# Kernel optimization log

Measured on AMD Instinct MI355X. Metric: run time of the kernel, lower is better.

Reference implementation:

```python
import jax, jax.numpy as jnp
import numpy as np
from jax.ops import segment_sum

N_NODES = 10000
N_EDGES = 320000


def leaky_relu(x):
    return jnp.where(x >= 0, x, 0.01 * x)


def gcn_layer(edge_h, src, dst, W, b):
    # (1) node h = mean of incoming edge features
    deg = segment_sum(jnp.ones((edge_h.shape[0],), edge_h.dtype), dst, num_segments=N_NODES)
    deg = jnp.maximum(deg, 1.0)
    h = segment_sum(edge_h, dst, num_segments=N_NODES) / deg[:, None]
    # (2) update_all: node h = sum over in-edges of src node h
    h2 = segment_sum(h[src], dst, num_segments=N_NODES)
    # (3) edge h = mean of endpoint node features
    eh = 0.5 * (h2[src] + h2[dst])
    # (4) linear on edge features
    return eh @ W.T + b


def setup_inputs() -> dict:
    key = jax.random.key(0)
    ks = jax.random.split(key, 20)
    d_in, d_h, d_out = 128, 256, 64
    inp = {
        'inputs1': jax.random.normal(ks[0], (N_EDGES, d_in), jnp.float32),
        'src1': jax.random.randint(ks[1], (N_EDGES,), 0, N_NODES, jnp.int32),
        'dst1': jax.random.randint(ks[2], (N_EDGES,), 0, N_NODES, jnp.int32),
        'inputs2': jax.random.normal(ks[3], (N_EDGES, d_in), jnp.float32),
        'src2': jax.random.randint(ks[4], (N_EDGES,), 0, N_NODES, jnp.int32),
        'dst2': jax.random.randint(ks[5], (N_EDGES,), 0, N_NODES, jnp.int32),
        'W11': jax.random.normal(ks[6], (d_h, d_in), jnp.float32) * 0.05,
        'b11': jax.random.normal(ks[7], (d_h,), jnp.float32) * 0.05,
        'W12': jax.random.normal(ks[8], (d_h, d_h), jnp.float32) * 0.05,
        'b12': jax.random.normal(ks[9], (d_h,), jnp.float32) * 0.05,
        'W21': jax.random.normal(ks[10], (d_h, d_in), jnp.float32) * 0.05,
        'b21': jax.random.normal(ks[11], (d_h,), jnp.float32) * 0.05,
        'W22': jax.random.normal(ks[12], (d_h, d_h), jnp.float32) * 0.05,
        'b22': jax.random.normal(ks[13], (d_h,), jnp.float32) * 0.05,
        'W3': jax.random.normal(ks[14], (d_out, 2 * d_h), jnp.float32) * 0.05,
        'b3': jax.random.normal(ks[15], (d_out,), jnp.float32) * 0.05,
    }
    return inp


def reference(inputs1, src1, dst1, inputs2, src2, dst2,
              W11, b11, W12, b12, W21, b21, W22, b22, W3, b3):
    h1 = leaky_relu(gcn_layer(inputs1, src1, dst1, W11, b11))
    h1 = leaky_relu(gcn_layer(h1, src1, dst1, W12, b12))
    h1 = jnp.mean(h1, axis=0)
    h2 = leaky_relu(gcn_layer(inputs2, src2, dst2, W21, b21))
    h2 = leaky_relu(gcn_layer(h2, src2, dst2, W22, b22))
    h2 = jnp.mean(h2, axis=0)
    out = jnp.concatenate((h1, h2), axis=0)
    return out @ W3.T + b3
```

## Files before the change

kernel.cpp:

```cpp
#include <hip/hip_runtime.h>
#include <cstddef>

#define NN 10000
#define NB 2500

typedef unsigned int u32;
typedef unsigned short u16;
typedef __attribute__((ext_vector_type(8))) short short8;
typedef __attribute__((ext_vector_type(4))) float f32x4;

__device__ __forceinline__ float lrelu(float x) { return x >= 0.f ? x : 0.01f * x; }

__device__ __forceinline__ float bf_lo(u32 v) { union { u32 i; float f; } c; c.i = v << 16; return c.f; }
__device__ __forceinline__ float bf_hi(u32 v) { union { u32 i; float f; } c; c.i = v & 0xFFFF0000u; return c.f; }
__device__ __forceinline__ u32 rne_bits(float f) {
  union { float f; u32 i; } c; c.f = f;
  return c.i + 0x7FFFu + ((c.i >> 16) & 1u);
}
__device__ __forceinline__ u32 pack2(float a, float b) {
  return (rne_bits(a) >> 16) | (rne_bits(b) & 0xFFFF0000u);
}

__global__ __launch_bounds__(256) void wconv_kernel(
    const float* __restrict__ a, const float* __restrict__ b,
    const float* __restrict__ c, const float* __restrict__ d,
    u16* __restrict__ oa, u16* __restrict__ ob,
    u16* __restrict__ oc, u16* __restrict__ od,
    int* __restrict__ degbase ) {
  int i = blockIdx.x * 256 + threadIdx.x;
  if (i < 32768) oa[i] = (u16)(rne_bits(a[i]) >> 16);
  else if (i < 98304) ob[i - 32768] = (u16)(rne_bits(b[i - 32768]) >> 16);
  else if (i < 131072) oc[i - 98304] = (u16)(rne_bits(c[i - 98304]) >> 16);
  else if (i < 196608) od[i - 131072] = (u16)(rne_bits(d[i - 131072]) >> 16);
  if (i < 4 * NN) degbase[i] = 0;
}

__global__ __launch_bounds__(256) void count_b_kernel(const int* __restrict__ dstA,
                                                      const int* __restrict__ dstB,
                                                      int* __restrict__ degbase, int E) {
  const int g = blockIdx.y;
  const int* dst = g ? dstB : dstA;
  int* degi = degbase + (size_t)g * 2 * NN;
  int e = blockIdx.x * 256 + threadIdx.x;
  if (e < E) atomicAdd(&degi[dst[e]], 1);
}

__global__ __launch_bounds__(1024) void scan_b_kernel(const int* __restrict__ degbase,
                                                      int* __restrict__ offbase,
                                                      float* __restrict__ rdegbase, int n) {
  const int g = blockIdx.x;
  const int* degi = degbase + (size_t)g * 2 * NN;
  int* off = offbase + (size_t)g * NN;
  float* rdeg = rdegbase + (size_t)g * NN;
  __shared__ int wsum[16];
  __shared__ int wpre[16];
  __shared__ int carry_s;
  const int tid = threadIdx.x;
  const int lane = tid & 63, w = tid >> 6;
  if (tid == 0) carry_s = 0;
  __syncthreads();
  for (int base = 0; base < n; base += 1024) {
    int i = base + tid;
    int x = (i < n) ? degi[i] : 0;
    int v = x;
#pragma unroll
    for (int d = 1; d < 64; d <<= 1) {
      int t = __shfl_up(v, d);
      if (lane >= d) v += t;
    }
    if (lane == 63) wsum[w] = v;
    __syncthreads();
    if (tid == 0) {
      int s = carry_s;
#pragma unroll
      for (int j = 0; j < 16; ++j) { int t = wsum[j]; wpre[j] = s; s += t; }
      carry_s = s;
    }
    __syncthreads();
    if (i < n) {
      off[i] = wpre[w] + (v - x);
      rdeg[i] = 1.0f / fmaxf((float)x, 1.0f);
    }
    __syncthreads();
  }
}

__global__ __launch_bounds__(256) void scatterA_b_kernel(
    const float* __restrict__ featA, const float* __restrict__ featB,
    const int* __restrict__ srcA, const int* __restrict__ dstA,
    const int* __restrict__ srcB, const int* __restrict__ dstB,
    const int* __restrict__ offbase, int* __restrict__ degbase,
    u32* __restrict__ tmpb , int* __restrict__ esrc_sb, int E) {
  const int g = blockIdx.y;
  const float* feat = g ? featB : featA;
  const int* src = g ? srcB : srcA;
  const int* dst = g ? dstB : dstA;
  const int* off = offbase + (size_t)g * NN;
  int* cursor = degbase + (size_t)g * 2 * NN + NN;
  u32* tmp = tmpb + (size_t)g * E * 64;
  int* esrc_s = esrc_sb + (size_t)g * E;
  const int idx = blockIdx.x * 8 + (threadIdx.x >> 5);
  const int lane32 = threadIdx.x & 31;
  if (idx >= E) return;
  int p0 = 0, sv = 0;
  if (lane32 == 0) {
    const int dv = dst[idx];
    sv = src[idx];
    p0 = off[dv] + atomicAdd(&cursor[dv], 1);
  }
  const int p = __shfl(p0, threadIdx.x & 32);
  const float4 v = *(const float4*)&feat[(size_t)idx * 128 + (lane32 << 2)];
  uint2 o;
  o.x = pack2(v.x, v.y);
  o.y = pack2(v.z, v.w);
  *(uint2*)&tmp[(size_t)p * 64 + (lane32 << 1)] = o;
  if (lane32 == 0) esrc_s[p] = sv;
}

__global__ __launch_bounds__(256) void reduceA_b_kernel(
    const u32* __restrict__ tmpb, const int* __restrict__ offbase,
    const int* __restrict__ degbase, const float* __restrict__ rdegbase,
    u32* __restrict__ outbfb , int E) {
  const int g = blockIdx.y;
  const u32* tmp = tmpb + (size_t)g * E * 64;
  const int* off = offbase + (size_t)g * NN;
  const int* degi = degbase + (size_t)g * 2 * NN;
  const float* rdeg = rdegbase + (size_t)g * NN;
  u32* outbf = outbfb + (size_t)g * NN * 64;
  const int n = (blockIdx.x << 2) + (threadIdx.x >> 6);
  const int lane = threadIdx.x & 63;
  const int hl = lane & 31, h = lane >> 5;
  const int o = off[n], d = degi[n];
  const u32* basep = tmp + (size_t)o * 64 + (hl << 1);
  float4 acc = make_float4(0.f, 0.f, 0.f, 0.f);
  int j = h;
  for (; j + 6 < d; j += 8) {
    const uint2 v0 = *(const uint2*)(basep + (size_t)j * 64);
    const uint2 v1 = *(const uint2*)(basep + (size_t)(j + 2) * 64);
    const uint2 v2 = *(const uint2*)(basep + (size_t)(j + 4) * 64);
    const uint2 v3 = *(const uint2*)(basep + (size_t)(j + 6) * 64);
    acc.x += (bf_lo(v0.x) + bf_lo(v1.x)) + (bf_lo(v2.x) + bf_lo(v3.x));
    acc.y += (bf_hi(v0.x) + bf_hi(v1.x)) + (bf_hi(v2.x) + bf_hi(v3.x));
    acc.z += (bf_lo(v0.y) + bf_lo(v1.y)) + (bf_lo(v2.y) + bf_lo(v3.y));
    acc.w += (bf_hi(v0.y) + bf_hi(v1.y)) + (bf_hi(v2.y) + bf_hi(v3.y));
  }
  for (; j < d; j += 2) {
    const uint2 v0 = *(const uint2*)(basep + (size_t)j * 64);
    acc.x += bf_lo(v0.x); acc.y += bf_hi(v0.x);
    acc.z += bf_lo(v0.y); acc.w += bf_hi(v0.y);
  }
  acc.x += __shfl(acc.x, lane ^ 32);
  acc.y += __shfl(acc.y, lane ^ 32);
  acc.z += __shfl(acc.z, lane ^ 32);
  acc.w += __shfl(acc.w, lane ^ 32);
  if (h == 0) {
    const float sc = rdeg[n];
    uint2 r;
    r.x = pack2(acc.x * sc, acc.y * sc);
    r.y = pack2(acc.z * sc, acc.w * sc);
    *(uint2*)&outbf[(size_t)n * 64 + (hl << 1)] = r;
  }
}

__global__ __launch_bounds__(256) void gatherB_b_kernel(
    const u32* __restrict__ featb , const int* __restrict__ gidxb,
    const int* __restrict__ offbase, const int* __restrict__ degbase,
    u32* __restrict__ outbfb, int E) {
  const int bid = blockIdx.x;
  const int r = bid & 7, t = bid >> 3;
  const int g = r >> 2;
  const int nb = t * 4 + (r & 3);
  const u32* feat = featb + (size_t)g * NN * 64;
  const int* gidx = gidxb + (size_t)g * E;
  const int* off = offbase + (size_t)g * NN;
  const int* degi = degbase + (size_t)g * 2 * NN;
  u32* outbf = outbfb + (size_t)g * NN * 64;
  const int n = (nb << 2) + (threadIdx.x >> 6);
  const int lane = threadIdx.x & 63;
  const int hl = lane & 31, h = lane >> 5;
  const int o = off[n], d = degi[n];
  const int fo = hl << 1;
  float4 acc = make_float4(0.f, 0.f, 0.f, 0.f);
  for (int c0 = 0; c0 < d; c0 += 64) {
    const int m = min(64, d - c0);
    const int gg = (lane < m) ? gidx[o + c0 + lane] : 0;
    const int pairs = m >> 1;
    int i = 0;
    for (; i + 4 <= pairs; i += 4) {
      const int e0 = 2 * i + h;
      const int s0 = __shfl(gg, e0), s1 = __shfl(gg, e0 + 2);
      const int s2 = __shfl(gg, e0 + 4), s3 = __shfl(gg, e0 + 6);
      const uint2 v0 = *(const uint2*)&feat[(s0 << 6) + fo];
      const uint2 v1 = *(const uint2*)&feat[(s1 << 6) + fo];
      const uint2 v2 = *(const uint2*)&feat[(s2 << 6) + fo];
      const uint2 v3 = *(const uint2*)&feat[(s3 << 6) + fo];
      acc.x += (bf_lo(v0.x) + bf_lo(v1.x)) + (bf_lo(v2.x) + bf_lo(v3.x));
      acc.y += (bf_hi(v0.x) + bf_hi(v1.x)) + (bf_hi(v2.x) + bf_hi(v3.x));
      acc.z += (bf_lo(v0.y) + bf_lo(v1.y)) + (bf_lo(v2.y) + bf_lo(v3.y));
      acc.w += (bf_hi(v0.y) + bf_hi(v1.y)) + (bf_hi(v2.y) + bf_hi(v3.y));
    }
    for (; i < pairs; ++i) {
      const int s0 = __shfl(gg, 2 * i + h);
      const uint2 v0 = *(const uint2*)&feat[(s0 << 6) + fo];
      acc.x += bf_lo(v0.x); acc.y += bf_hi(v0.x);
      acc.z += bf_lo(v0.y); acc.w += bf_hi(v0.y);
    }
    if (m & 1) {
      const int s0 = __shfl(gg, m - 1);
      const float wgt = (h == 0) ? 1.f : 0.f;
      const uint2 v0 = *(const uint2*)&feat[(s0 << 6) + fo];
      acc.x = fmaf(bf_lo(v0.x), wgt, acc.x);
      acc.y = fmaf(bf_hi(v0.x), wgt, acc.y);
      acc.z = fmaf(bf_lo(v0.y), wgt, acc.z);
      acc.w = fmaf(bf_hi(v0.y), wgt, acc.w);
    }
  }
  acc.x += __shfl(acc.x, lane ^ 32);
  acc.y += __shfl(acc.y, lane ^ 32);
  acc.z += __shfl(acc.z, lane ^ 32);
  acc.w += __shfl(acc.w, lane ^ 32);
  if (h == 0) {
    uint2 r2;
    r2.x = pack2(acc.x, acc.y);
    r2.y = pack2(acc.z, acc.w);
    *(uint2*)&outbf[(size_t)n * 64 + (hl << 1)] = r2;
  }
}

__device__ __forceinline__ void acc_bf4(float4& a, uint2 v, const float4& zn, const float4& bb) {
  a.x += lrelu(0.5f * (bf_lo(v.x) + zn.x) + bb.x);
  a.y += lrelu(0.5f * (bf_hi(v.x) + zn.y) + bb.y);
  a.z += lrelu(0.5f * (bf_lo(v.y) + zn.z) + bb.z);
  a.w += lrelu(0.5f * (bf_hi(v.y) + zn.w) + bb.w);
}

__global__ __launch_bounds__(256) void passC_b_kernel(
    const u32* __restrict__ Zb_, const int* __restrict__ esrcb,
    const int* __restrict__ offbase, const int* __restrict__ degbase,
    const float* __restrict__ rdegbase,
    const float* __restrict__ biasA, const float* __restrict__ biasB,
    u32* __restrict__ hBb, int E) {
  const int bid = blockIdx.x;
  const int r = bid & 7, t = bid >> 3;
  const int g = r >> 2, fh = (r >> 1) & 1;
  const int nb = t * 2 + (r & 1);
  const u32* Z = Zb_ + (size_t)g * NN * 128;
  const int* esrc = esrcb + (size_t)g * E;
  const int* off = offbase + (size_t)g * NN;
  const int* degi = degbase + (size_t)g * 2 * NN;
  const float* rdeg = rdegbase + (size_t)g * NN;
  const float* bias = g ? biasB : biasA;
  u32* hB = hBb + (size_t)g * NN * 128;
  const int n = (nb << 2) + (threadIdx.x >> 6);
  const int lane = threadIdx.x & 63;
  const int hl = lane & 31, h = lane >> 5;
  const int o = off[n], d = degi[n];
  const int fo = (fh << 6) + (hl << 1);
  const uint2 znv = *(const uint2*)&Z[(n << 7) + fo];
  const float4 zn = make_float4(bf_lo(znv.x), bf_hi(znv.x), bf_lo(znv.y), bf_hi(znv.y));
  const float4 bb = *(const float4*)&bias[(fh << 7) + (hl << 2)];
  float4 a = make_float4(0.f, 0.f, 0.f, 0.f);
  for (int c0 = 0; c0 < d; c0 += 64) {
    const int m = min(64, d - c0);
    const int gg = (lane < m) ? esrc[o + c0 + lane] : 0;
    const int pairs = m >> 1;
    int i = 0;
    for (; i + 4 <= pairs; i += 4) {
      const int e0 = 2 * i + h;
      const int s0 = __shfl(gg, e0), s1 = __shfl(gg, e0 + 2);
      const int s2 = __shfl(gg, e0 + 4), s3 = __shfl(gg, e0 + 6);
      const uint2 z0 = *(const uint2*)&Z[(s0 << 7) + fo];
      const uint2 z1 = *(const uint2*)&Z[(s1 << 7) + fo];
      const uint2 z2 = *(const uint2*)&Z[(s2 << 7) + fo];
      const uint2 z3 = *(const uint2*)&Z[(s3 << 7) + fo];
      acc_bf4(a, z0, zn, bb);
      acc_bf4(a, z1, zn, bb);
      acc_bf4(a, z2, zn, bb);
      acc_bf4(a, z3, zn, bb);
    }
    for (; i < pairs; ++i) {
      const int s0 = __shfl(gg, 2 * i + h);
      const uint2 z0 = *(const uint2*)&Z[(s0 << 7) + fo];
      acc_bf4(a, z0, zn, bb);
    }
    if (m & 1) {
      const int s0 = __shfl(gg, m - 1);
      const uint2 z0 = *(const uint2*)&Z[(s0 << 7) + fo];
      if (h == 0) acc_bf4(a, z0, zn, bb);
    }
  }
  a.x += __shfl(a.x, lane ^ 32); a.y += __shfl(a.y, lane ^ 32);
  a.z += __shfl(a.z, lane ^ 32); a.w += __shfl(a.w, lane ^ 32);
  if (h == 0) {
    const float rr = rdeg[n];
    uint2 outv;
    outv.x = pack2(a.x * rr, a.y * rr);
    outv.y = pack2(a.z * rr, a.w * rr);
    *(uint2*)&hB[(n << 7) + fo] = outv;
  }
}

__global__ __launch_bounds__(256) void gatherC_b_kernel(
    const u32* __restrict__ featb , const int* __restrict__ gidxb,
    const int* __restrict__ offbase, const int* __restrict__ degbase,
    u32* __restrict__ outbfb, int E) {
  const int bid = blockIdx.x;
  const int r = bid & 7, t = bid >> 3;
  const int g = r >> 2, fh = (r >> 1) & 1;
  const int nb = t * 2 + (r & 1);
  const u32* feat = featb + (size_t)g * NN * 128;
  const int* gidx = gidxb + (size_t)g * E;
  const int* off = offbase + (size_t)g * NN;
  const int* degi = degbase + (size_t)g * 2 * NN;
  u32* outbf = outbfb + (size_t)g * NN * 128;
  const int n = (nb << 2) + (threadIdx.x >> 6);
  const int lane = threadIdx.x & 63;
  const int hl = lane & 31, h = lane >> 5;
  const int o = off[n], d = degi[n];
  const int fo = (fh << 6) + (hl << 1);
  float4 a = make_float4(0.f, 0.f, 0.f, 0.f);
  for (int c0 = 0; c0 < d; c0 += 64) {
    const int m = min(64, d - c0);
    const int gg = (lane < m) ? gidx[o + c0 + lane] : 0;
    const int pairs = m >> 1;
    int i = 0;
    for (; i + 4 <= pairs; i += 4) {
      const int e0 = 2 * i + h;
      const int s0 = __shfl(gg, e0), s1 = __shfl(gg, e0 + 2);
      const int s2 = __shfl(gg, e0 + 4), s3 = __shfl(gg, e0 + 6);
      const uint2 z0 = *(const uint2*)&feat[(s0 << 7) + fo];
      const uint2 z1 = *(const uint2*)&feat[(s1 << 7) + fo];
      const uint2 z2 = *(const uint2*)&feat[(s2 << 7) + fo];
      const uint2 z3 = *(const uint2*)&feat[(s3 << 7) + fo];
      a.x += (bf_lo(z0.x) + bf_lo(z1.x)) + (bf_lo(z2.x) + bf_lo(z3.x));
      a.y += (bf_hi(z0.x) + bf_hi(z1.x)) + (bf_hi(z2.x) + bf_hi(z3.x));
      a.z += (bf_lo(z0.y) + bf_lo(z1.y)) + (bf_lo(z2.y) + bf_lo(z3.y));
      a.w += (bf_hi(z0.y) + bf_hi(z1.y)) + (bf_hi(z2.y) + bf_hi(z3.y));
    }
    for (; i < pairs; ++i) {
      const int s0 = __shfl(gg, 2 * i + h);
      const uint2 z0 = *(const uint2*)&feat[(s0 << 7) + fo];
      a.x += bf_lo(z0.x); a.y += bf_hi(z0.x);
      a.z += bf_lo(z0.y); a.w += bf_hi(z0.y);
    }
    if (m & 1) {
      const int s0 = __shfl(gg, m - 1);
      const uint2 z0 = *(const uint2*)&feat[(s0 << 7) + fo];
      if (h == 0) {
        a.x += bf_lo(z0.x); a.y += bf_hi(z0.x);
        a.z += bf_lo(z0.y); a.w += bf_hi(z0.y);
      }
    }
  }
  a.x += __shfl(a.x, lane ^ 32); a.y += __shfl(a.y, lane ^ 32);
  a.z += __shfl(a.z, lane ^ 32); a.w += __shfl(a.w, lane ^ 32);
  if (h == 0) {
    uint2 outv;
    outv.x = pack2(a.x, a.y);
    outv.y = pack2(a.z, a.w);
    *(uint2*)&outbf[(n << 7) + fo] = outv;
  }
}

__global__ __launch_bounds__(256) void passE_b_kernel(
    const u32* __restrict__ Z2b, const int* __restrict__ esrcb,
    const int* __restrict__ offbase, const int* __restrict__ degbase,
    const float* __restrict__ biasA, const float* __restrict__ biasB,
    float* __restrict__ partialsb , int nNodes, int E) {
  const int bid = blockIdx.x;
  const int r = bid & 7, t = bid >> 3;
  const int g = r >> 2, fh = (r >> 1) & 1;
  const int blk = t * 2 + (r & 1);
  const u32* Z2 = Z2b + (size_t)g * NN * 128;
  const int* esrc = esrcb + (size_t)g * E;
  const int* off = offbase + (size_t)g * NN;
  const int* degi = degbase + (size_t)g * 2 * NN;
  const float* bias = g ? biasB : biasA;
  float* partials = partialsb + (size_t)((g * 2 + fh) * 128 + blk) * 128;
  const int lane = threadIdx.x & 63, w = threadIdx.x >> 6;
  const int hl = lane & 31, h = lane >> 5;
  const int fo = (fh << 6) + (hl << 1);
  const float4 bb = *(const float4*)&bias[(fh << 7) + (hl << 2)];
  float4 a = make_float4(0.f, 0.f, 0.f, 0.f);
  for (int n = blk * 4 + w; n < nNodes; n += 512) {
    const int o = off[n], d = degi[n];
    const uint2 znv = *(const uint2*)&Z2[(n << 7) + fo];
    const float4 zn = make_float4(bf_lo(znv.x), bf_hi(znv.x), bf_lo(znv.y), bf_hi(znv.y));
    for (int c0 = 0; c0 < d; c0 += 64) {
      const int m = min(64, d - c0);
      const int gg = (lane < m) ? esrc[o + c0 + lane] : 0;
      const int pairs = m >> 1;
      int i = 0;
      for (; i + 4 <= pairs; i += 4) {
        const int e0 = 2 * i + h;
        const int s0 = __shfl(gg, e0), s1 = __shfl(gg, e0 + 2);
        const int s2 = __shfl(gg, e0 + 4), s3 = __shfl(gg, e0 + 6);
        const uint2 z0 = *(const uint2*)&Z2[(s0 << 7) + fo];
        const uint2 z1 = *(const uint2*)&Z2[(s1 << 7) + fo];
        const uint2 z2 = *(const uint2*)&Z2[(s2 << 7) + fo];
        const uint2 z3 = *(const uint2*)&Z2[(s3 << 7) + fo];
        acc_bf4(a, z0, zn, bb);
        acc_bf4(a, z1, zn, bb);
        acc_bf4(a, z2, zn, bb);
        acc_bf4(a, z3, zn, bb);
      }
      for (; i < pairs; ++i) {
        const int s0 = __shfl(gg, 2 * i + h);
        const uint2 z0 = *(const uint2*)&Z2[(s0 << 7) + fo];
        acc_bf4(a, z0, zn, bb);
      }
      if (m & 1) {
        const int s0 = __shfl(gg, m - 1);
        const uint2 z0 = *(const uint2*)&Z2[(s0 << 7) + fo];
        if (h == 0) acc_bf4(a, z0, zn, bb);
      }
    }
  }
  a.x += __shfl(a.x, lane ^ 32); a.y += __shfl(a.y, lane ^ 32);
  a.z += __shfl(a.z, lane ^ 32); a.w += __shfl(a.w, lane ^ 32);
  __shared__ float red[4][128];
  if (h == 0) *(float4*)&red[w][hl << 2] = a;
  __syncthreads();
  const int tid = threadIdx.x;
  if (tid < 128) partials[tid] = red[0][tid] + red[1][tid] + red[2][tid] + red[3][tid];
}

__global__ __launch_bounds__(1024) void final_fused_kernel(
    const float* __restrict__ partialsb ,
    const float* __restrict__ W3, const float* __restrict__ b3,
    float* __restrict__ out, float invE) {
  __shared__ float smacc[512];
  __shared__ float tmp2[2][512];
  __shared__ float red[16][64];
  const int tid = threadIdx.x;
  {
    const int half = tid >> 9;
    const int q = tid & 511;
    const float* basep = partialsb + (size_t)(q >> 7) * 128 * 128 + (q & 127);
    float s = 0.f;
    for (int b = half * 64; b < half * 64 + 64; ++b) s += basep[(size_t)b * 128];
    tmp2[half][q] = s;
  }
  __syncthreads();
  if (tid < 512) smacc[tid] = tmp2[0][tid] + tmp2[1][tid];
  __syncthreads();
  const int j = tid & 63, part = tid >> 6;
  float acc = 0.f;
  for (int kk = 0; kk < 32; ++kk) {
    const int k = part * 32 + kk;
    acc += smacc[k] * W3[(size_t)j * 512 + k];
  }
  red[part][j] = acc;
  __syncthreads();
  if (part == 0) {
    float s = 0.f;
#pragma unroll
    for (int p = 0; p < 16; ++p) s += red[p][j];
    out[j] = b3[j] + s * invE;
  }
}

template <int K>
__global__ __launch_bounds__(256) void gemm_mfma_b_kernel(const u16* __restrict__ Ab,
                                                          const u16* __restrict__ WA,
                                                          const u16* __restrict__ WB,
                                                          u16* __restrict__ Cb, int N) {
  const int g = blockIdx.z;
  const u16* A = Ab + (size_t)g * NN * K;
  const u16* Wb = g ? WB : WA;
  u16* C = Cb + (size_t)g * NN * 256;
  const int lane = threadIdx.x & 63;
  const int w = threadIdx.x >> 6;
  const int wm = w >> 1, wn = w & 1;
  const int bn = blockIdx.x * 64 + wm * 32;
  const int bo = blockIdx.y * 64 + wn * 32;
  const int r0 = lane & 15;
  const int kq = lane >> 4;
  const int ra0 = min(bn + r0, N - 1);
  const int ra1 = min(bn + 16 + r0, N - 1);
  const u16* a0p = &A[(size_t)ra0 * K + kq * 8];
  const u16* a1p = &A[(size_t)ra1 * K + kq * 8];
  const u16* b0p = &Wb[(size_t)(bo + r0) * K + kq * 8];
  const u16* b1p = &Wb[(size_t)(bo + 16 + r0) * K + kq * 8];
  f32x4 acc00 = {0.f, 0.f, 0.f, 0.f}, acc01 = {0.f, 0.f, 0.f, 0.f};
  f32x4 acc10 = {0.f, 0.f, 0.f, 0.f}, acc11 = {0.f, 0.f, 0.f, 0.f};
#pragma unroll
  for (int k0 = 0; k0 < K; k0 += 32) {
    const short8 a0 = *(const short8*)(a0p + k0);
    const short8 a1 = *(const short8*)(a1p + k0);
    const short8 b0 = *(const short8*)(b0p + k0);
    const short8 b1 = *(const short8*)(b1p + k0);
    acc00 = __builtin_amdgcn_mfma_f32_16x16x32_bf16(a0, b0, acc00, 0, 0, 0);
    acc01 = __builtin_amdgcn_mfma_f32_16x16x32_bf16(a0, b1, acc01, 0, 0, 0);
    acc10 = __builtin_amdgcn_mfma_f32_16x16x32_bf16(a1, b0, acc10, 0, 0, 0);
    acc11 = __builtin_amdgcn_mfma_f32_16x16x32_bf16(a1, b1, acc11, 0, 0, 0);
  }
#pragma unroll
  for (int r = 0; r < 4; ++r) {
    const int n0 = bn + 4 * kq + r;
    if (n0 < N) {
      C[(size_t)n0 * 256 + bo + r0] = (u16)(rne_bits(acc00[r]) >> 16);
      C[(size_t)n0 * 256 + bo + 16 + r0] = (u16)(rne_bits(acc01[r]) >> 16);
    }
    const int n1 = bn + 16 + 4 * kq + r;
    if (n1 < N) {
      C[(size_t)n1 * 256 + bo + r0] = (u16)(rne_bits(acc10[r]) >> 16);
      C[(size_t)n1 * 256 + bo + 16 + r0] = (u16)(rne_bits(acc11[r]) >> 16);
    }
  }
}

extern "C" void kernel_launch(void* const* d_in, const int* in_sizes, int n_in,
                              void* d_out, int out_size, void* d_ws, size_t ws_size,
                              hipStream_t stream) {
  const float* in1 = (const float*)d_in[0];
  const int* src1 = (const int*)d_in[1];
  const int* dst1 = (const int*)d_in[2];
  const float* in2 = (const float*)d_in[3];
  const int* src2 = (const int*)d_in[4];
  const int* dst2 = (const int*)d_in[5];
  const float* W11 = (const float*)d_in[6];
  const float* b11 = (const float*)d_in[7];
  const float* W12 = (const float*)d_in[8];
  const float* b12 = (const float*)d_in[9];
  const float* W21 = (const float*)d_in[10];
  const float* b21 = (const float*)d_in[11];
  const float* W22 = (const float*)d_in[12];
  const float* b22 = (const float*)d_in[13];
  const float* W3 = (const float*)d_in[14];
  const float* b3 = (const float*)d_in[15];
  const int E = in_sizes[1];
  const int N = NN;

  char* base = (char*)d_ws;
  size_t pos = 0;
  auto carve = [&](size_t bytes) -> char* {
    char* p = base + pos;
    pos = (pos + bytes + 511) & ~(size_t)511;
    return p;
  };
  int* degbase = (int*)carve((size_t)2 * 2 * N * sizeof(int));
  int* offb = (int*)carve((size_t)2 * N * sizeof(int));
  float* rdegb = (float*)carve((size_t)2 * N * sizeof(float));
  int* esrc_sb = (int*)carve((size_t)2 * E * sizeof(int));
  u32* tmpb = (u32*)carve((size_t)2 * E * 64 * sizeof(u32));
  u32* Hb = (u32*)carve((size_t)2 * N * 64 * sizeof(u32));
  u32* H2b = (u32*)carve((size_t)2 * N * 64 * sizeof(u32));
  u32* Zb = (u32*)carve((size_t)2 * N * 128 * sizeof(u32));
  u32* HBb = (u32*)carve((size_t)2 * N * 128 * sizeof(u32));
  u32* H2Bb = (u32*)carve((size_t)2 * N * 128 * sizeof(u32));
  u16* Wa1 = (u16*)carve((size_t)32768 * sizeof(u16));
  u16* Wb1 = (u16*)carve((size_t)65536 * sizeof(u16));
  u16* Wa2 = (u16*)carve((size_t)32768 * sizeof(u16));
  u16* Wb2 = (u16*)carve((size_t)65536 * sizeof(u16));
  float* partialsb = (float*)carve((size_t)2 * 2 * 128 * 128 * sizeof(float));
  (void)ws_size; (void)n_in; (void)out_size;

  const int EB = (E + 255) / 256;
  const dim3 g2(EB, 2);
  const dim3 gemm_grid((N + 63) / 64, 4, 2);

  wconv_kernel<<<768, 256, 0, stream>>>(W11, W12, W21, W22, Wa1, Wb1, Wa2, Wb2, degbase);

  count_b_kernel<<<g2, 256, 0, stream>>>(dst1, dst2, degbase, E);
  scan_b_kernel<<<2, 1024, 0, stream>>>(degbase, offb, rdegb, N);

  scatterA_b_kernel<<<dim3((E + 7) / 8, 2), 256, 0, stream>>>(
      in1, in2, src1, dst1, src2, dst2, offb, degbase, tmpb, esrc_sb, E);
  reduceA_b_kernel<<<dim3(NB, 2), 256, 0, stream>>>(tmpb, offb, degbase, rdegb, Hb, E);

  gatherB_b_kernel<<<2 * NB, 256, 0, stream>>>(Hb, esrc_sb, offb, degbase, H2b, E);
  gemm_mfma_b_kernel<128><<<gemm_grid, 256, 0, stream>>>((const u16*)H2b, Wa1, Wa2, (u16*)Zb, N);

  passC_b_kernel<<<4 * NB, 256, 0, stream>>>(Zb, esrc_sb, offb, degbase, rdegb, b11, b21, HBb, E);
  gatherC_b_kernel<<<4 * NB, 256, 0, stream>>>(HBb, esrc_sb, offb, degbase, H2Bb, E);
  gemm_mfma_b_kernel<256><<<gemm_grid, 256, 0, stream>>>((const u16*)H2Bb, Wb1, Wb2, (u16*)Zb, N);

  passE_b_kernel<<<512, 256, 0, stream>>>(Zb, esrc_sb, offb, degbase, b12, b22, partialsb, N, E);
  final_fused_kernel<<<1, 1024, 0, stream>>>(partialsb, W3, b3, (float*)d_out, 1.0f / (float)E);
}
```

Baseline: 395.3 us.

## Replace scatter-then-reduce of edge features with index sort and direct gather

The old path converted every edge feature row to bf16 and scattered it into a dst-sorted temporary buffer, then reduced that buffer per node. The new path only scatters edge ids and source ids into dst-sorted order, and the per-node reduction gathers fp32 rows straight from the original input by edge id. This removes the write and re-read of a large intermediate buffer at the cost of random-row fp32 reads in the reduction. Summation now runs on fp32 inputs instead of bf16-rounded ones.

```diff
diff --git a/kernel.cpp b/kernel.cpp
--- a/kernel.cpp
+++ b/kernel.cpp
@@ -85,44 +85,38 @@
   }
 }
 
-__global__ __launch_bounds__(256) void scatterA_b_kernel(
-    const float* __restrict__ featA, const float* __restrict__ featB,
-    const int* __restrict__ srcA, const int* __restrict__ dstA,
-    const int* __restrict__ srcB, const int* __restrict__ dstB,
-    const int* __restrict__ offbase, int* __restrict__ degbase,
-    u32* __restrict__ tmpb , int* __restrict__ esrc_sb, int E) {
+__global__ __launch_bounds__(256) void fill_b_kernel(const int* __restrict__ srcA,
+                                                     const int* __restrict__ dstA,
+                                                     const int* __restrict__ srcB,
+                                                     const int* __restrict__ dstB,
+                                                     const int* __restrict__ offbase,
+                                                     int* __restrict__ degbase,
+                                                     int* __restrict__ eid_sb,
+                                                     int* __restrict__ esrc_sb, int E) {
   const int g = blockIdx.y;
-  const float* feat = g ? featB : featA;
   const int* src = g ? srcB : srcA;
   const int* dst = g ? dstB : dstA;
   const int* off = offbase + (size_t)g * NN;
   int* cursor = degbase + (size_t)g * 2 * NN + NN;
-  u32* tmp = tmpb + (size_t)g * E * 64;
+  int* eid_s = eid_sb + (size_t)g * E;
   int* esrc_s = esrc_sb + (size_t)g * E;
-  const int idx = blockIdx.x * 8 + (threadIdx.x >> 5);
-  const int lane32 = threadIdx.x & 31;
-  if (idx >= E) return;
-  int p0 = 0, sv = 0;
-  if (lane32 == 0) {
-    const int dv = dst[idx];
-    sv = src[idx];
-    p0 = off[dv] + atomicAdd(&cursor[dv], 1);
-  }
-  const int p = __shfl(p0, threadIdx.x & 32);
-  const float4 v = *(const float4*)&feat[(size_t)idx * 128 + (lane32 << 2)];
-  uint2 o;
-  o.x = pack2(v.x, v.y);
-  o.y = pack2(v.z, v.w);
-  *(uint2*)&tmp[(size_t)p * 64 + (lane32 << 1)] = o;
-  if (lane32 == 0) esrc_s[p] = sv;
-}
-
-__global__ __launch_bounds__(256) void reduceA_b_kernel(
-    const u32* __restrict__ tmpb, const int* __restrict__ offbase,
+  int e = blockIdx.x * 256 + threadIdx.x;
+  if (e < E) {
+    int d = dst[e];
+    int p = off[d] + atomicAdd(&cursor[d], 1);
+    eid_s[p] = e;
+    esrc_s[p] = src[e];
+  }
+}
+
+__global__ __launch_bounds__(256) void gatherA_b_kernel(
+    const float* __restrict__ featA, const float* __restrict__ featB,
+    const int* __restrict__ gidxb, const int* __restrict__ offbase,
     const int* __restrict__ degbase, const float* __restrict__ rdegbase,
     u32* __restrict__ outbfb , int E) {
   const int g = blockIdx.y;
-  const u32* tmp = tmpb + (size_t)g * E * 64;
+  const float* feat = g ? featB : featA;
+  const int* gidx = gidxb + (size_t)g * E;
   const int* off = offbase + (size_t)g * NN;
   const int* degi = degbase + (size_t)g * 2 * NN;
   const float* rdeg = rdegbase + (size_t)g * NN;
@@ -131,23 +125,40 @@
   const int lane = threadIdx.x & 63;
   const int hl = lane & 31, h = lane >> 5;
   const int o = off[n], d = degi[n];
-  const u32* basep = tmp + (size_t)o * 64 + (hl << 1);
+  const int fo = hl << 2;
   float4 acc = make_float4(0.f, 0.f, 0.f, 0.f);
-  int j = h;
-  for (; j + 6 < d; j += 8) {
-    const uint2 v0 = *(const uint2*)(basep + (size_t)j * 64);
-    const uint2 v1 = *(const uint2*)(basep + (size_t)(j + 2) * 64);
-    const uint2 v2 = *(const uint2*)(basep + (size_t)(j + 4) * 64);
-    const uint2 v3 = *(const uint2*)(basep + (size_t)(j + 6) * 64);
-    acc.x += (bf_lo(v0.x) + bf_lo(v1.x)) + (bf_lo(v2.x) + bf_lo(v3.x));
-    acc.y += (bf_hi(v0.x) + bf_hi(v1.x)) + (bf_hi(v2.x) + bf_hi(v3.x));
-    acc.z += (bf_lo(v0.y) + bf_lo(v1.y)) + (bf_lo(v2.y) + bf_lo(v3.y));
-    acc.w += (bf_hi(v0.y) + bf_hi(v1.y)) + (bf_hi(v2.y) + bf_hi(v3.y));
-  }
-  for (; j < d; j += 2) {
-    const uint2 v0 = *(const uint2*)(basep + (size_t)j * 64);
-    acc.x += bf_lo(v0.x); acc.y += bf_hi(v0.x);
-    acc.z += bf_lo(v0.y); acc.w += bf_hi(v0.y);
+  for (int c0 = 0; c0 < d; c0 += 64) {
+    const int m = min(64, d - c0);
+    const int gg = (lane < m) ? gidx[o + c0 + lane] : 0;
+    const int pairs = m >> 1;
+    int i = 0;
+    for (; i + 4 <= pairs; i += 4) {
+      const int e0 = 2 * i + h;
+      const int s0 = __shfl(gg, e0), s1 = __shfl(gg, e0 + 2);
+      const int s2 = __shfl(gg, e0 + 4), s3 = __shfl(gg, e0 + 6);
+      const float4 v0 = *(const float4*)&feat[(s0 << 7) + fo];
+      const float4 v1 = *(const float4*)&feat[(s1 << 7) + fo];
+      const float4 v2 = *(const float4*)&feat[(s2 << 7) + fo];
+      const float4 v3 = *(const float4*)&feat[(s3 << 7) + fo];
+      acc.x += (v0.x + v1.x) + (v2.x + v3.x);
+      acc.y += (v0.y + v1.y) + (v2.y + v3.y);
+      acc.z += (v0.z + v1.z) + (v2.z + v3.z);
+      acc.w += (v0.w + v1.w) + (v2.w + v3.w);
+    }
+    for (; i < pairs; ++i) {
+      const int s0 = __shfl(gg, 2 * i + h);
+      const float4 v0 = *(const float4*)&feat[(s0 << 7) + fo];
+      acc.x += v0.x; acc.y += v0.y; acc.z += v0.z; acc.w += v0.w;
+    }
+    if (m & 1) {
+      const int s0 = __shfl(gg, m - 1);
+      const float wgt = (h == 0) ? 1.f : 0.f;
+      const float4 v0 = *(const float4*)&feat[(s0 << 7) + fo];
+      acc.x = fmaf(v0.x, wgt, acc.x);
+      acc.y = fmaf(v0.y, wgt, acc.y);
+      acc.z = fmaf(v0.z, wgt, acc.z);
+      acc.w = fmaf(v0.w, wgt, acc.w);
+    }
   }
   acc.x += __shfl(acc.x, lane ^ 32);
   acc.y += __shfl(acc.y, lane ^ 32);
@@ -542,8 +553,8 @@
   int* degbase = (int*)carve((size_t)2 * 2 * N * sizeof(int));
   int* offb = (int*)carve((size_t)2 * N * sizeof(int));
   float* rdegb = (float*)carve((size_t)2 * N * sizeof(float));
+  int* eid_sb = (int*)carve((size_t)2 * E * sizeof(int));
   int* esrc_sb = (int*)carve((size_t)2 * E * sizeof(int));
-  u32* tmpb = (u32*)carve((size_t)2 * E * 64 * sizeof(u32));
   u32* Hb = (u32*)carve((size_t)2 * N * 64 * sizeof(u32));
   u32* H2b = (u32*)carve((size_t)2 * N * 64 * sizeof(u32));
   u32* Zb = (u32*)carve((size_t)2 * N * 128 * sizeof(u32));
@@ -558,17 +569,16 @@
 
   const int EB = (E + 255) / 256;
   const dim3 g2(EB, 2);
+  const dim3 n2(NB, 2);
   const dim3 gemm_grid((N + 63) / 64, 4, 2);
 
   wconv_kernel<<<768, 256, 0, stream>>>(W11, W12, W21, W22, Wa1, Wb1, Wa2, Wb2, degbase);
 
   count_b_kernel<<<g2, 256, 0, stream>>>(dst1, dst2, degbase, E);
   scan_b_kernel<<<2, 1024, 0, stream>>>(degbase, offb, rdegb, N);
-
-  scatterA_b_kernel<<<dim3((E + 7) / 8, 2), 256, 0, stream>>>(
-      in1, in2, src1, dst1, src2, dst2, offb, degbase, tmpb, esrc_sb, E);
-  reduceA_b_kernel<<<dim3(NB, 2), 256, 0, stream>>>(tmpb, offb, degbase, rdegb, Hb, E);
-
+  fill_b_kernel<<<g2, 256, 0, stream>>>(src1, dst1, src2, dst2, offb, degbase, eid_sb, esrc_sb, E);
+
+  gatherA_b_kernel<<<n2, 256, 0, stream>>>(in1, in2, eid_sb, offb, degbase, rdegb, Hb, E);
   gatherB_b_kernel<<<2 * NB, 256, 0, stream>>>(Hb, esrc_sb, offb, degbase, H2b, E);
   gemm_mfma_b_kernel<128><<<gemm_grid, 256, 0, stream>>>((const u16*)H2b, Wa1, Wa2, (u16*)Zb, N);
 
```

After: 353.4 us. 10.6% less time.
